# Performance work log

Measured on AMD Instinct MI355X. Metric: run time of the kernel, lower is better.

## Reference

```python
import jax, jax.numpy as jnp
import numpy as np

DN = ('NDHWC', 'DHWIO', 'NDHWC')
EPS = 1e-5  # torch BatchNorm default

def _conv(x, w, s):
    # Minkowski conv, kernel 3 centered: output coord j gathers input coords s*j + {-1,0,1}
    return jax.lax.conv_general_dilated(x, w, (s, s, s), ((1, 1),) * 3, dimension_numbers=DN)

def _convt(x, w):
    # stride-2 transpose conv, kernel 3 centered: output p gets input c where 2c in {p-1,p,p+1}
    return jax.lax.conv_general_dilated(x, w, (1, 1, 1), ((1, 2),) * 3,
                                        lhs_dilation=(2, 2, 2), dimension_numbers=DN)

def _down(m):
    # stride-2 coordinate map: a coarse voxel is active iff any of its 2x2x2 fine voxels is
    B, G = m.shape[0], m.shape[1]
    return m.reshape(B, G // 2, 2, G // 2, 2, G // 2, 2).any(axis=(2, 4, 6))

def _mbn(h, m, g, b):
    # MinkowskiBatchNorm: BatchNorm1d over the active (sparse) feature rows only
    mf = m[..., None].astype(h.dtype)
    h = h * mf
    cnt = jnp.maximum(jnp.sum(mf), 1.0)
    mean = jnp.sum(h, axis=(0, 1, 2, 3)) / cnt
    var = jnp.sum(((h - mean) * mf) ** 2, axis=(0, 1, 2, 3)) / cnt
    return ((h - mean) * jax.lax.rsqrt(var + EPS) * g + b) * mf


def setup_inputs() -> dict:
    key = jax.random.key(0)
    ks = jax.random.split(key, 8)
    B, G, Cin, Cout = 2, 64, 4, 16
    def w(k, shape, fan):
        return jax.random.normal(k, shape, jnp.float32) * np.float32(1.0 / np.sqrt(fan))
    return {
        'x': jax.random.normal(ks[0], (B, G, G, G, Cin), jnp.float32),
        'mask': jax.random.bernoulli(ks[1], 0.1, (B, G, G, G)),
        'w1': w(ks[2], (3, 3, 3, Cin, 8), 27 * Cin), 'g1': jnp.ones(8), 'b1': jnp.zeros(8),
        'w2': w(ks[3], (3, 3, 3, 8, 16), 27 * 8), 'g2': jnp.ones(16), 'b2': jnp.zeros(16),
        'w3': w(ks[4], (3, 3, 3, 16, 32), 27 * 16), 'g3': jnp.ones(32), 'b3': jnp.zeros(32),
        'w3t': w(ks[5], (3, 3, 3, 32, 16), 27 * 32), 'g3t': jnp.ones(16), 'b3t': jnp.zeros(16),
        'w2t': w(ks[6], (3, 3, 3, 32, 16), 27 * 32), 'g2t': jnp.ones(16), 'b2t': jnp.zeros(16),
        'w1x1': w(ks[7], (24, Cout), 24),
    }


def reference(x, mask, w1, g1, b1, w2, g2, b2, w3, g3, b3,
              w3t, g3t, b3t, w2t, g2t, b2t, w1x1):
    m1 = mask
    m2 = _down(m1)
    m4 = _down(m2)
    mf1 = m1[..., None].astype(x.dtype)

    xs = x * mf1                                      # sparse tensor: zero at inactive coords
    s1 = _mbn(_conv(xs, w1, 1), m1, g1, b1)           # block1, stride 1
    o = jax.nn.relu(s1)
    s2 = _mbn(_conv(o, w2, 2), m2, g2, b2)            # block2, stride 2
    o = jax.nn.relu(s2)
    s4 = _mbn(_conv(o, w3, 2), m4, g3, b3)            # block3, stride 4
    o = jax.nn.relu(s4)

    o = jax.nn.relu(_mbn(_convt(o, w3t), m2, g3t, b3t))   # block3_tr -> stride-2 coords
    o = jnp.concatenate([o, s2], axis=-1)                 # ME.cat(out, out_s2) -> 32 ch
    o = jax.nn.relu(_mbn(_convt(o, w2t), m1, g2t, b2t))   # block2_tr -> stride-1 coords
    o = jnp.concatenate([o, s1], axis=-1)                 # ME.cat(out, out_s1) -> 24 ch
    return jnp.einsum('bdhwc,co->bdhwo', o, w1x1) * mf1   # conv1_tr: 1x1x1 conv
```

## Files before the change

kernel.cpp:

```cpp
#include <hip/hip_runtime.h>

#define NVOX1 524288
#define NVOX2 65536
#define NVOX4 8192

#define ST_SUM1 16
#define ST_SQ1  24
#define ST_SUM2 32
#define ST_SQ2  48
#define ST_SUM3 64
#define ST_SQ3  96
#define ST_SUM3T 128
#define ST_SQ3T  144
#define ST_SUM2T 160
#define ST_SQ2T  176
#define FLAG_OFF 200
#define IC_N1 204
#define IC_N2 205
#define IC_N4 206
#define ST_ZERO 256

#define OFF_M1C 512
#define OFF_M2  (OFF_M1C + NVOX1)
#define OFF_M4  (OFF_M2 + NVOX2)
#define OFF_H1  (OFF_M4 + NVOX4)
#define OFF_S2  (OFF_H1 + NVOX1 * 8)
#define OFF_H3  (OFF_S2 + NVOX2 * 16)
#define OFF_T3  (OFF_H3 + NVOX4 * 32)
#define OFF_L1  (OFF_T3 + NVOX2 * 16)
#define OFF_L2  (OFF_L1 + NVOX1)
#define OFF_L4  (OFF_L2 + NVOX2)
#define OFF_BC1 (OFF_L4 + NVOX4)
#define OFF_BC2 (OFF_BC1 + 2048)
#define OFF_BC4 (OFF_BC2 + 256)

#define EPSBN 1e-5f

template <int C>
__device__ __forceinline__ void wreduce(float& a, float& b) {
#pragma unroll
  for (int off = C; off < 64; off <<= 1) {
    a += __shfl_xor(a, off, 64);
    b += __shfl_xor(b, off, 64);
  }
}

__device__ __forceinline__ int taps1d(int p, int gin, int* c, int* k) {
  if ((p & 1) == 0) { c[0] = p >> 1; k[0] = 1; return 1; }
  int n = 0;
  c[n] = (p - 1) >> 1; k[n] = 0; n++;
  int c2 = (p + 1) >> 1;
  if (c2 < gin) { c[n] = c2; k[n] = 2; n++; }
  return n;
}

__global__ __launch_bounds__(256) void k_detect(const unsigned int* __restrict__ m,
                                                int* __restrict__ flags) {
  int tid = blockIdx.x * 256 + threadIdx.x;
  int hasf = 0, hasb = 0;
  for (int i = tid; i < NVOX1; i += 256 * 256) {
    unsigned int v = m[i];
    if (v == 0x3F800000u) hasf = 1;
    else if (v > 1u) hasb = 1;
  }
  hasf = __syncthreads_or(hasf);
  hasb = __syncthreads_or(hasb);
  if (threadIdx.x == 0) {
    if (hasf) atomicOr(&flags[0], 1);
    if (hasb) atomicOr(&flags[1], 1);
  }
}

__global__ __launch_bounds__(256) void k_canon(const void* __restrict__ mraw,
                                               int* __restrict__ m1c,
                                               const int* __restrict__ flags,
                                               int* __restrict__ blkcnt1) {
  int idx = blockIdx.x * 256 + threadIdx.x;
  int isf = flags[0], isb = flags[1];
  int v;
  if (isf)      v = (((const float*)mraw)[idx] != 0.f);
  else if (isb) v = (((const unsigned char*)mraw)[idx] != 0);
  else          v = (((const int*)mraw)[idx] != 0);
  m1c[idx] = v;
  int c = __syncthreads_count(v);
  if (threadIdx.x == 0) blkcnt1[blockIdx.x] = c;
}

__global__ __launch_bounds__(256) void k_down1(const int* __restrict__ m1,
                                               int* __restrict__ m2,
                                               int* __restrict__ blkcnt2) {
  int idx = blockIdx.x * 256 + threadIdx.x;
  int x = idx & 31, y = (idx >> 5) & 31, z = (idx >> 10) & 31, b = idx >> 15;
  int any = 0;
#pragma unroll
  for (int dz = 0; dz < 2; dz++)
#pragma unroll
    for (int dy = 0; dy < 2; dy++)
#pragma unroll
      for (int dx = 0; dx < 2; dx++)
        any |= m1[((b * 64 + 2 * z + dz) * 64 + 2 * y + dy) * 64 + 2 * x + dx];
  any = any ? 1 : 0;
  m2[idx] = any;
  int c = __syncthreads_count(any);
  if (threadIdx.x == 0) blkcnt2[blockIdx.x] = c;
}

__global__ __launch_bounds__(256) void k_down2(const int* __restrict__ m2,
                                               int* __restrict__ m4,
                                               int* __restrict__ blkcnt4) {
  int idx = blockIdx.x * 256 + threadIdx.x;
  int x = idx & 15, y = (idx >> 4) & 15, z = (idx >> 8) & 15, b = idx >> 12;
  int any = 0;
#pragma unroll
  for (int dz = 0; dz < 2; dz++)
#pragma unroll
    for (int dy = 0; dy < 2; dy++)
#pragma unroll
      for (int dx = 0; dx < 2; dx++)
        any |= m2[((b * 32 + 2 * z + dz) * 32 + 2 * y + dy) * 32 + 2 * x + dx];
  any = any ? 1 : 0;
  m4[idx] = any;
  int c = __syncthreads_count(any);
  if (threadIdx.x == 0) blkcnt4[blockIdx.x] = c;
}

__global__ __launch_bounds__(1024) void k_scan(int* __restrict__ bc1,
                                               int* __restrict__ bc2,
                                               int* __restrict__ bc4,
                                               int* __restrict__ cnts) {
  __shared__ int sA[2048], sB[2048];
  int* a; int n; int outIdx;
  if (blockIdx.x == 0)      { a = bc1; n = 2048; outIdx = IC_N1; }
  else if (blockIdx.x == 1) { a = bc2; n = 256;  outIdx = IC_N2; }
  else                      { a = bc4; n = 32;   outIdx = IC_N4; }
  int t = threadIdx.x;
  int i0 = t, i1 = t + 1024;
  int v0 = (i0 < n) ? a[i0] : 0;
  int v1 = (i1 < n) ? a[i1] : 0;
  sA[i0] = v0; sA[i1] = v1;
  __syncthreads();
  int* src = sA; int* dst = sB;
  for (int st = 1; st < 2048; st <<= 1) {
    int x0 = src[i0]; if (i0 >= st) x0 += src[i0 - st];
    int x1 = src[i1]; if (i1 >= st) x1 += src[i1 - st];
    dst[i0] = x0; dst[i1] = x1;
    __syncthreads();
    int* tmp = src; src = dst; dst = tmp;
  }
  if (i0 < n) a[i0] = src[i0] - v0;
  if (i1 < n) a[i1] = src[i1] - v1;
  if (t == 0) cnts[outIdx] = src[2047];
}

__global__ __launch_bounds__(256) void k_scatter(const int* __restrict__ m1,
                                                 const int* __restrict__ m2,
                                                 const int* __restrict__ m4,
                                                 const int* __restrict__ bc1,
                                                 const int* __restrict__ bc2,
                                                 const int* __restrict__ bc4,
                                                 int* __restrict__ list1,
                                                 int* __restrict__ list2,
                                                 int* __restrict__ list4) {
  __shared__ int s_w[4];
  int bid = blockIdx.x, t = threadIdx.x;
  const int* mask; const int* base; int* list; int lb;
  if (bid < 2048)      { mask = m1; base = bc1; list = list1; lb = bid; }
  else if (bid < 2304) { mask = m2; base = bc2; list = list2; lb = bid - 2048; }
  else                 { mask = m4; base = bc4; list = list4; lb = bid - 2304; }
  int idx = lb * 256 + t;
  int act = mask[idx];
  unsigned long long b = __ballot(act != 0);
  int lane = t & 63, wid = t >> 6;
  if (lane == 0) s_w[wid] = __popcll(b);
  __syncthreads();
  int wbase = 0;
  for (int i = 0; i < wid; i++) wbase += s_w[i];
  if (act) {
    int pre = __popcll(b & ((1ull << lane) - 1ull));
    list[base[lb] + wbase + pre] = idx;
  }
}

__global__ __launch_bounds__(256) void k_conv1(const float* __restrict__ x,
                                               const int* __restrict__ m1,
                                               const int* __restrict__ list1,
                                               const int* __restrict__ cnts,
                                               const float* __restrict__ w,
                                               float* __restrict__ h1,
                                               float* __restrict__ stats) {
  __shared__ float s_w[27 * 36];
  __shared__ float s_sum[8], s_sq[8];
  int t = threadIdx.x;
  { const float4* w4 = (const float4*)w;
    for (int i = t; i < 216; i += 256) {
      int flat = i * 4, tap = flat >> 5, rem = flat & 31;
      *(float4*)(s_w + tap * 36 + rem) = w4[i];
    } }
  if (t < 8) { s_sum[t] = 0.f; s_sq[t] = 0.f; }
  __syncthreads();
  int items = cnts[IC_N1] * 8;
  float sum = 0.f, sq = 0.f;
  for (int i = blockIdx.x * 256 + t; i < items; i += gridDim.x * 256) {
    int li = i >> 3, co = i & 7;
    int v = list1[li];
    int vx = v & 63, vy = (v >> 6) & 63, vz = (v >> 12) & 63, vb = v >> 18;
    float a0 = 0.f, a1 = 0.f;
    for (int kd = 0; kd < 3; kd++) { int d = vz + kd - 1; if ((unsigned)d >= 64u) continue;
      for (int kh = 0; kh < 3; kh++) { int h = vy + kh - 1; if ((unsigned)h >= 64u) continue;
        for (int kw = 0; kw < 3; kw++) { int ww = vx + kw - 1; if ((unsigned)ww >= 64u) continue;
          int ni = ((vb * 64 + d) * 64 + h) * 64 + ww;
          if (!m1[ni]) continue;
          float4 ip = *(const float4*)(x + (size_t)ni * 4);
          const float* wp = s_w + ((kd * 3 + kh) * 3 + kw) * 36 + co;
          a0 = fmaf(ip.x, wp[0], a0);
          a1 = fmaf(ip.y, wp[8], a1);
          a0 = fmaf(ip.z, wp[16], a0);
          a1 = fmaf(ip.w, wp[24], a1);
        } } }
    float acc = a0 + a1;
    h1[(size_t)v * 8 + co] = acc;
    sum += acc; sq += acc * acc;
  }
  wreduce<8>(sum, sq);
  if ((t & 63) < 8) { atomicAdd(&s_sum[t & 7], sum); atomicAdd(&s_sq[t & 7], sq); }
  __syncthreads();
  if (t < 8) {
    if (s_sum[t] != 0.f) atomicAdd(&stats[ST_SUM1 + t], s_sum[t]);
    if (s_sq[t]  != 0.f) atomicAdd(&stats[ST_SQ1 + t], s_sq[t]);
  }
}

__global__ __launch_bounds__(256) void k_conv2(const float* __restrict__ h1,
                                               const int* __restrict__ m1,
                                               const int* __restrict__ list2,
                                               const int* __restrict__ cnts,
                                               const float* __restrict__ w,
                                               const float* __restrict__ g1,
                                               const float* __restrict__ b1,
                                               float* __restrict__ s2,
                                               float* __restrict__ stats) {
  __shared__ float s_w[27 * 132];
  __shared__ float s_sc[8], s_bi[8];
  __shared__ float s_sum[16], s_sq[16];
  int t = threadIdx.x;
  { const float4* w4 = (const float4*)w;
    for (int i = t; i < 864; i += 256) {
      int flat = i * 4, tap = flat >> 7, rem = flat & 127;
      *(float4*)(s_w + tap * 132 + rem) = w4[i];
    } }
  if (t < 8) {
    float cnt = fmaxf((float)cnts[IC_N1], 1.f);
    float mean = stats[ST_SUM1 + t] / cnt;
    float var = fmaxf(stats[ST_SQ1 + t] / cnt - mean * mean, 0.f);
    float sc = g1[t] * rsqrtf(var + EPSBN);
    s_sc[t] = sc; s_bi[t] = b1[t] - mean * sc;
  }
  if (t < 16) { s_sum[t] = 0.f; s_sq[t] = 0.f; }
  __syncthreads();
  int items = cnts[IC_N2] * 16;
  float sum = 0.f, sq = 0.f;
  for (int i = blockIdx.x * 256 + t; i < items; i += gridDim.x * 256) {
    int li = i >> 4, co = i & 15;
    int v = list2[li];
    int vx = v & 31, vy = (v >> 5) & 31, vz = (v >> 10) & 31, vb = v >> 15;
    float a0 = 0.f, a1 = 0.f;
    for (int kd = 0; kd < 3; kd++) { int d = 2 * vz + kd - 1; if ((unsigned)d >= 64u) continue;
      for (int kh = 0; kh < 3; kh++) { int h = 2 * vy + kh - 1; if ((unsigned)h >= 64u) continue;
        for (int kw = 0; kw < 3; kw++) { int ww = 2 * vx + kw - 1; if ((unsigned)ww >= 64u) continue;
          int ni = ((vb * 64 + d) * 64 + h) * 64 + ww;
          if (!m1[ni]) continue;
          float4 i0 = *(const float4*)(h1 + (size_t)ni * 8);
          float4 i1 = *(const float4*)(h1 + (size_t)ni * 8 + 4);
          const float* wp = s_w + ((kd * 3 + kh) * 3 + kw) * 132 + co;
          float vv;
          vv = fmaxf(fmaf(i0.x, s_sc[0], s_bi[0]), 0.f); a0 = fmaf(vv, wp[0 * 16], a0);
          vv = fmaxf(fmaf(i0.y, s_sc[1], s_bi[1]), 0.f); a1 = fmaf(vv, wp[1 * 16], a1);
          vv = fmaxf(fmaf(i0.z, s_sc[2], s_bi[2]), 0.f); a0 = fmaf(vv, wp[2 * 16], a0);
          vv = fmaxf(fmaf(i0.w, s_sc[3], s_bi[3]), 0.f); a1 = fmaf(vv, wp[3 * 16], a1);
          vv = fmaxf(fmaf(i1.x, s_sc[4], s_bi[4]), 0.f); a0 = fmaf(vv, wp[4 * 16], a0);
          vv = fmaxf(fmaf(i1.y, s_sc[5], s_bi[5]), 0.f); a1 = fmaf(vv, wp[5 * 16], a1);
          vv = fmaxf(fmaf(i1.z, s_sc[6], s_bi[6]), 0.f); a0 = fmaf(vv, wp[6 * 16], a0);
          vv = fmaxf(fmaf(i1.w, s_sc[7], s_bi[7]), 0.f); a1 = fmaf(vv, wp[7 * 16], a1);
        } } }
    float acc = a0 + a1;
    s2[(size_t)v * 16 + co] = acc;
    sum += acc; sq += acc * acc;
  }
  wreduce<16>(sum, sq);
  if ((t & 63) < 16) { atomicAdd(&s_sum[t & 15], sum); atomicAdd(&s_sq[t & 15], sq); }
  __syncthreads();
  if (t < 16) {
    if (s_sum[t] != 0.f) atomicAdd(&stats[ST_SUM2 + t], s_sum[t]);
    if (s_sq[t]  != 0.f) atomicAdd(&stats[ST_SQ2 + t], s_sq[t]);
  }
}

__global__ __launch_bounds__(512) void k_conv3(const float* __restrict__ s2raw,
                                               const int* __restrict__ m2,
                                               const int* __restrict__ list4,
                                               const int* __restrict__ cnts,
                                               const float* __restrict__ w,
                                               const float* __restrict__ g2,
                                               const float* __restrict__ b2,
                                               float* __restrict__ h3,
                                               float* __restrict__ stats) {
  __shared__ float s_w[27 * 516];
  __shared__ float s_sc[16], s_bi[16];
  __shared__ float s_sum[32], s_sq[32];
  int t = threadIdx.x;
  { const float4* w4 = (const float4*)w;
    for (int i = t; i < 3456; i += 512) {
      int flat = i * 4, tap = flat >> 9, rem = flat & 511;
      *(float4*)(s_w + tap * 516 + rem) = w4[i];
    } }
  if (t < 16) {
    float cnt = fmaxf((float)cnts[IC_N2], 1.f);
    float mean = stats[ST_SUM2 + t] / cnt;
    float var = fmaxf(stats[ST_SQ2 + t] / cnt - mean * mean, 0.f);
    float sc = g2[t] * rsqrtf(var + EPSBN);
    s_sc[t] = sc; s_bi[t] = b2[t] - mean * sc;
  }
  if (t < 32) { s_sum[t] = 0.f; s_sq[t] = 0.f; }
  __syncthreads();
  int items = cnts[IC_N4] * 32;
  float sum = 0.f, sq = 0.f;
  for (int i = blockIdx.x * 512 + t; i < items; i += gridDim.x * 512) {
    int li = i >> 5, co = i & 31;
    int v = list4[li];
    int vx = v & 15, vy = (v >> 4) & 15, vz = (v >> 8) & 15, vb = v >> 12;
    float ac[4] = {0.f, 0.f, 0.f, 0.f};
    for (int kd = 0; kd < 3; kd++) { int d = 2 * vz + kd - 1; if ((unsigned)d >= 32u) continue;
      for (int kh = 0; kh < 3; kh++) { int h = 2 * vy + kh - 1; if ((unsigned)h >= 32u) continue;
        for (int kw = 0; kw < 3; kw++) { int ww = 2 * vx + kw - 1; if ((unsigned)ww >= 32u) continue;
          int ni = ((vb * 32 + d) * 32 + h) * 32 + ww;
          if (!m2[ni]) continue;
          const float4* ip = (const float4*)(s2raw + (size_t)ni * 16);
          const float* wp = s_w + ((kd * 3 + kh) * 3 + kw) * 516 + co;
#pragma unroll
          for (int cq = 0; cq < 4; cq++) {
            float4 q = ip[cq];
            float vv;
            vv = fmaxf(fmaf(q.x, s_sc[cq * 4 + 0], s_bi[cq * 4 + 0]), 0.f); ac[0] = fmaf(vv, wp[(cq * 4 + 0) * 32], ac[0]);
            vv = fmaxf(fmaf(q.y, s_sc[cq * 4 + 1], s_bi[cq * 4 + 1]), 0.f); ac[1] = fmaf(vv, wp[(cq * 4 + 1) * 32], ac[1]);
            vv = fmaxf(fmaf(q.z, s_sc[cq * 4 + 2], s_bi[cq * 4 + 2]), 0.f); ac[2] = fmaf(vv, wp[(cq * 4 + 2) * 32], ac[2]);
            vv = fmaxf(fmaf(q.w, s_sc[cq * 4 + 3], s_bi[cq * 4 + 3]), 0.f); ac[3] = fmaf(vv, wp[(cq * 4 + 3) * 32], ac[3]);
          }
        } } }
    float acc = (ac[0] + ac[1]) + (ac[2] + ac[3]);
    h3[(size_t)v * 32 + co] = acc;
    sum += acc; sq += acc * acc;
  }
  wreduce<32>(sum, sq);
  if ((t & 63) < 32) { atomicAdd(&s_sum[t & 31], sum); atomicAdd(&s_sq[t & 31], sq); }
  __syncthreads();
  if (t < 32) {
    if (s_sum[t] != 0.f) atomicAdd(&stats[ST_SUM3 + t], s_sum[t]);
    if (s_sq[t]  != 0.f) atomicAdd(&stats[ST_SQ3 + t], s_sq[t]);
  }
}

__global__ __launch_bounds__(512) void k_convt3(const float* __restrict__ h3raw,
                                                const int* __restrict__ m4,
                                                const int* __restrict__ list2,
                                                const int* __restrict__ cnts,
                                                const float* __restrict__ w,
                                                const float* __restrict__ g3,
                                                const float* __restrict__ b3,
                                                float* __restrict__ t3,
                                                float* __restrict__ stats) {
  __shared__ float s_w[27 * 516];
  __shared__ float s_sc[32], s_bi[32];
  __shared__ float s_sum[16], s_sq[16];
  int t = threadIdx.x;
  { const float4* w4 = (const float4*)w;
    for (int i = t; i < 3456; i += 512) {
      int flat = i * 4, tap = flat >> 9, rem = flat & 511;
      *(float4*)(s_w + tap * 516 + rem) = w4[i];
    } }
  if (t < 32) {
    float cnt = fmaxf((float)cnts[IC_N4], 1.f);
    float mean = stats[ST_SUM3 + t] / cnt;
    float var = fmaxf(stats[ST_SQ3 + t] / cnt - mean * mean, 0.f);
    float sc = g3[t] * rsqrtf(var + EPSBN);
    s_sc[t] = sc; s_bi[t] = b3[t] - mean * sc;
  }
  if (t < 16) { s_sum[t] = 0.f; s_sq[t] = 0.f; }
  __syncthreads();
  int items = cnts[IC_N2] * 16;
  float sum = 0.f, sq = 0.f;
  for (int i = blockIdx.x * 512 + t; i < items; i += gridDim.x * 512) {
    int li = i >> 4, co = i & 15;
    int v = list2[li];
    int px = v & 31, py = (v >> 5) & 31, pz = (v >> 10) & 31, vb = v >> 15;
    int cz[2], kz[2], cy[2], ky[2], cx[2], kx[2];
    int nz = taps1d(pz, 16, cz, kz);
    int ny = taps1d(py, 16, cy, ky);
    int nx = taps1d(px, 16, cx, kx);
    float ac[4] = {0.f, 0.f, 0.f, 0.f};
    for (int iz = 0; iz < nz; iz++)
      for (int iy = 0; iy < ny; iy++)
        for (int ix = 0; ix < nx; ix++) {
          int ni = ((vb * 16 + cz[iz]) * 16 + cy[iy]) * 16 + cx[ix];
          if (!m4[ni]) continue;
          const float4* ip = (const float4*)(h3raw + (size_t)ni * 32);
          const float* wp = s_w + ((kz[iz] * 3 + ky[iy]) * 3 + kx[ix]) * 516 + co;
#pragma unroll
          for (int cq = 0; cq < 8; cq++) {
            float4 q = ip[cq];
            float vv;
            vv = fmaxf(fmaf(q.x, s_sc[cq * 4 + 0], s_bi[cq * 4 + 0]), 0.f); ac[0] = fmaf(vv, wp[(cq * 4 + 0) * 16], ac[0]);
            vv = fmaxf(fmaf(q.y, s_sc[cq * 4 + 1], s_bi[cq * 4 + 1]), 0.f); ac[1] = fmaf(vv, wp[(cq * 4 + 1) * 16], ac[1]);
            vv = fmaxf(fmaf(q.z, s_sc[cq * 4 + 2], s_bi[cq * 4 + 2]), 0.f); ac[2] = fmaf(vv, wp[(cq * 4 + 2) * 16], ac[2]);
            vv = fmaxf(fmaf(q.w, s_sc[cq * 4 + 3], s_bi[cq * 4 + 3]), 0.f); ac[3] = fmaf(vv, wp[(cq * 4 + 3) * 16], ac[3]);
          }
        }
    float acc = (ac[0] + ac[1]) + (ac[2] + ac[3]);
    t3[(size_t)v * 16 + co] = acc;
    sum += acc; sq += acc * acc;
  }
  wreduce<16>(sum, sq);
  if ((t & 63) < 16) { atomicAdd(&s_sum[t & 15], sum); atomicAdd(&s_sq[t & 15], sq); }
  __syncthreads();
  if (t < 16) {
    if (s_sum[t] != 0.f) atomicAdd(&stats[ST_SUM3T + t], s_sum[t]);
    if (s_sq[t]  != 0.f) atomicAdd(&stats[ST_SQ3T + t], s_sq[t]);
  }
}

__global__ __launch_bounds__(512) void k_convt2(const float* __restrict__ t3raw,
                                                const float* __restrict__ s2raw,
                                                const int* __restrict__ m2,
                                                const int* __restrict__ list1,
                                                const int* __restrict__ cnts,
                                                const float* __restrict__ w,
                                                const float* __restrict__ g3t,
                                                const float* __restrict__ b3t,
                                                const float* __restrict__ g2,
                                                const float* __restrict__ b2,
                                                float* __restrict__ outraw,
                                                float* __restrict__ stats) {
  __shared__ float s_w[27 * 516];
  __shared__ float s_sct[16], s_bit[16], s_sc2[16], s_bi2[16];
  __shared__ float s_sum[16], s_sq[16];
  int t = threadIdx.x;
  { const float4* w4 = (const float4*)w;
    for (int i = t; i < 3456; i += 512) {
      int flat = i * 4, tap = flat >> 9, rem = flat & 511;
      *(float4*)(s_w + tap * 516 + rem) = w4[i];
    } }
  if (t < 16) {
    float cnt = fmaxf((float)cnts[IC_N2], 1.f);
    float mean = stats[ST_SUM3T + t] / cnt;
    float var = fmaxf(stats[ST_SQ3T + t] / cnt - mean * mean, 0.f);
    float sc = g3t[t] * rsqrtf(var + EPSBN);
    s_sct[t] = sc; s_bit[t] = b3t[t] - mean * sc;
    float mean2 = stats[ST_SUM2 + t] / cnt;
    float var2 = fmaxf(stats[ST_SQ2 + t] / cnt - mean2 * mean2, 0.f);
    float sc2 = g2[t] * rsqrtf(var2 + EPSBN);
    s_sc2[t] = sc2; s_bi2[t] = b2[t] - mean2 * sc2;
    s_sum[t] = 0.f; s_sq[t] = 0.f;
  }
  __syncthreads();
  int items = cnts[IC_N1] * 16;
  float sum = 0.f, sq = 0.f;
  for (int i = blockIdx.x * 512 + t; i < items; i += gridDim.x * 512) {
    int li = i >> 4, co = i & 15;
    int v = list1[li];
    int px = v & 63, py = (v >> 6) & 63, pz = (v >> 12) & 63, vb = v >> 18;
    int cz[2], kz[2], cy[2], ky[2], cx[2], kx[2];
    int nz = taps1d(pz, 32, cz, kz);
    int ny = taps1d(py, 32, cy, ky);
    int nx = taps1d(px, 32, cx, kx);
    float ac[4] = {0.f, 0.f, 0.f, 0.f};
    for (int iz = 0; iz < nz; iz++)
      for (int iy = 0; iy < ny; iy++)
        for (int ix = 0; ix < nx; ix++) {
          int ni = ((vb * 32 + cz[iz]) * 32 + cy[iy]) * 32 + cx[ix];
          if (!m2[ni]) continue;
          const float4* tp = (const float4*)(t3raw + (size_t)ni * 16);
          const float4* sp = (const float4*)(s2raw + (size_t)ni * 16);
          const float* wp = s_w + ((kz[iz] * 3 + ky[iy]) * 3 + kx[ix]) * 516 + co;
#pragma unroll
          for (int cq = 0; cq < 4; cq++) {
            float4 q = tp[cq];
            float vv;
            vv = fmaxf(fmaf(q.x, s_sct[cq * 4 + 0], s_bit[cq * 4 + 0]), 0.f); ac[0] = fmaf(vv, wp[(cq * 4 + 0) * 16], ac[0]);
            vv = fmaxf(fmaf(q.y, s_sct[cq * 4 + 1], s_bit[cq * 4 + 1]), 0.f); ac[1] = fmaf(vv, wp[(cq * 4 + 1) * 16], ac[1]);
            vv = fmaxf(fmaf(q.z, s_sct[cq * 4 + 2], s_bit[cq * 4 + 2]), 0.f); ac[2] = fmaf(vv, wp[(cq * 4 + 2) * 16], ac[2]);
            vv = fmaxf(fmaf(q.w, s_sct[cq * 4 + 3], s_bit[cq * 4 + 3]), 0.f); ac[3] = fmaf(vv, wp[(cq * 4 + 3) * 16], ac[3]);
          }
#pragma unroll
          for (int cq = 0; cq < 4; cq++) {
            float4 q = sp[cq];
            float vv;
            vv = fmaf(q.x, s_sc2[cq * 4 + 0], s_bi2[cq * 4 + 0]); ac[0] = fmaf(vv, wp[(16 + cq * 4 + 0) * 16], ac[0]);
            vv = fmaf(q.y, s_sc2[cq * 4 + 1], s_bi2[cq * 4 + 1]); ac[1] = fmaf(vv, wp[(16 + cq * 4 + 1) * 16], ac[1]);
            vv = fmaf(q.z, s_sc2[cq * 4 + 2], s_bi2[cq * 4 + 2]); ac[2] = fmaf(vv, wp[(16 + cq * 4 + 2) * 16], ac[2]);
            vv = fmaf(q.w, s_sc2[cq * 4 + 3], s_bi2[cq * 4 + 3]); ac[3] = fmaf(vv, wp[(16 + cq * 4 + 3) * 16], ac[3]);
          }
        }
    float acc = (ac[0] + ac[1]) + (ac[2] + ac[3]);
    outraw[(size_t)v * 16 + co] = acc;
    sum += acc; sq += acc * acc;
  }
  wreduce<16>(sum, sq);
  if ((t & 63) < 16) { atomicAdd(&s_sum[t & 15], sum); atomicAdd(&s_sq[t & 15], sq); }
  __syncthreads();
  if (t < 16) {
    if (s_sum[t] != 0.f) atomicAdd(&stats[ST_SUM2T + t], s_sum[t]);
    if (s_sq[t]  != 0.f) atomicAdd(&stats[ST_SQ2T + t], s_sq[t]);
  }
}

__global__ __launch_bounds__(256) void k_final(float* __restrict__ out,
                                               const float* __restrict__ h1raw,
                                               const int* __restrict__ list1,
                                               const int* __restrict__ cnts,
                                               const float* __restrict__ g2t,
                                               const float* __restrict__ b2t,
                                               const float* __restrict__ g1,
                                               const float* __restrict__ b1,
                                               const float* __restrict__ w1x1,
                                               const float* __restrict__ stats) {
  __shared__ float s_sc[16], s_bi[16], s_sc1[8], s_bi1[8], s_w[384];
  int t = threadIdx.x;
  for (int i = t; i < 384; i += 256) s_w[i] = w1x1[i];
  if (t < 16) {
    float cnt = fmaxf((float)cnts[IC_N1], 1.f);
    float mean = stats[ST_SUM2T + t] / cnt;
    float var = fmaxf(stats[ST_SQ2T + t] / cnt - mean * mean, 0.f);
    float sc = g2t[t] * rsqrtf(var + EPSBN);
    s_sc[t] = sc; s_bi[t] = b2t[t] - mean * sc;
  }
  if (t < 8) {
    float cnt = fmaxf((float)cnts[IC_N1], 1.f);
    float mean = stats[ST_SUM1 + t] / cnt;
    float var = fmaxf(stats[ST_SQ1 + t] / cnt - mean * mean, 0.f);
    float sc = g1[t] * rsqrtf(var + EPSBN);
    s_sc1[t] = sc; s_bi1[t] = b1[t] - mean * sc;
  }
  __syncthreads();
  int n = cnts[IC_N1];
  for (int i = blockIdx.x * 256 + t; i < n; i += gridDim.x * 256) {
    int v = list1[i];
    float* op = out + (size_t)v * 16;
    float t2[16];
    {
      const float4* op4 = (const float4*)op;
#pragma unroll
      for (int cq = 0; cq < 4; cq++) {
        float4 q = op4[cq];
        t2[cq * 4 + 0] = fmaxf(fmaf(q.x, s_sc[cq * 4 + 0], s_bi[cq * 4 + 0]), 0.f);
        t2[cq * 4 + 1] = fmaxf(fmaf(q.y, s_sc[cq * 4 + 1], s_bi[cq * 4 + 1]), 0.f);
        t2[cq * 4 + 2] = fmaxf(fmaf(q.z, s_sc[cq * 4 + 2], s_bi[cq * 4 + 2]), 0.f);
        t2[cq * 4 + 3] = fmaxf(fmaf(q.w, s_sc[cq * 4 + 3], s_bi[cq * 4 + 3]), 0.f);
      }
    }
    float s1v[8];
    {
      const float4* sp4 = (const float4*)(h1raw + (size_t)v * 8);
#pragma unroll
      for (int cq = 0; cq < 2; cq++) {
        float4 q = sp4[cq];
        s1v[cq * 4 + 0] = fmaf(q.x, s_sc1[cq * 4 + 0], s_bi1[cq * 4 + 0]);
        s1v[cq * 4 + 1] = fmaf(q.y, s_sc1[cq * 4 + 1], s_bi1[cq * 4 + 1]);
        s1v[cq * 4 + 2] = fmaf(q.z, s_sc1[cq * 4 + 2], s_bi1[cq * 4 + 2]);
        s1v[cq * 4 + 3] = fmaf(q.w, s_sc1[cq * 4 + 3], s_bi1[cq * 4 + 3]);
      }
    }
    float o[16];
#pragma unroll
    for (int oc = 0; oc < 16; oc++) o[oc] = 0.f;
#pragma unroll
    for (int c = 0; c < 16; c++) {
      float vv = t2[c];
#pragma unroll
      for (int oc = 0; oc < 16; oc++) o[oc] = fmaf(vv, s_w[c * 16 + oc], o[oc]);
    }
#pragma unroll
    for (int c = 0; c < 8; c++) {
      float vv = s1v[c];
#pragma unroll
      for (int oc = 0; oc < 16; oc++) o[oc] = fmaf(vv, s_w[(16 + c) * 16 + oc], o[oc]);
    }
    float4* op4 = (float4*)op;
#pragma unroll
    for (int cq = 0; cq < 4; cq++) {
      float4 q = {o[cq * 4 + 0], o[cq * 4 + 1], o[cq * 4 + 2], o[cq * 4 + 3]};
      op4[cq] = q;
    }
  }
}

extern "C" void kernel_launch(void* const* d_in, const int* in_sizes, int n_in,
                              void* d_out, int out_size, void* d_ws, size_t ws_size,
                              hipStream_t stream) {
  const float* x    = (const float*)d_in[0];
  const void*  mraw = d_in[1];
  const float* w1   = (const float*)d_in[2];
  const float* g1   = (const float*)d_in[3];
  const float* b1   = (const float*)d_in[4];
  const float* w2   = (const float*)d_in[5];
  const float* g2   = (const float*)d_in[6];
  const float* b2   = (const float*)d_in[7];
  const float* w3   = (const float*)d_in[8];
  const float* g3   = (const float*)d_in[9];
  const float* b3   = (const float*)d_in[10];
  const float* w3t  = (const float*)d_in[11];
  const float* g3t  = (const float*)d_in[12];
  const float* b3t  = (const float*)d_in[13];
  const float* w2t  = (const float*)d_in[14];
  const float* g2t  = (const float*)d_in[15];
  const float* b2t  = (const float*)d_in[16];
  const float* w1x1 = (const float*)d_in[17];

  float* ws = (float*)d_ws;
  float* stats = ws;
  int* cnts = (int*)ws;
  int* flags = (int*)(ws + FLAG_OFF);
  int* m1c = (int*)(ws + OFF_M1C);
  int* m2  = (int*)(ws + OFF_M2);
  int* m4  = (int*)(ws + OFF_M4);
  float* h1 = ws + OFF_H1;
  float* s2 = ws + OFF_S2;
  float* h3 = ws + OFF_H3;
  float* t3 = ws + OFF_T3;
  int* list1 = (int*)(ws + OFF_L1);
  int* list2 = (int*)(ws + OFF_L2);
  int* list4 = (int*)(ws + OFF_L4);
  int* bc1 = (int*)(ws + OFF_BC1);
  int* bc2 = (int*)(ws + OFF_BC2);
  int* bc4 = (int*)(ws + OFF_BC4);
  float* out = (float*)d_out;

  hipMemsetAsync(ws, 0, ST_ZERO * sizeof(float), stream);
  hipMemsetAsync(d_out, 0, (size_t)out_size * sizeof(float), stream);
  k_detect<<<256, 256, 0, stream>>>((const unsigned int*)mraw, flags);
  k_canon<<<NVOX1 / 256, 256, 0, stream>>>(mraw, m1c, flags, bc1);
  k_down1<<<NVOX2 / 256, 256, 0, stream>>>(m1c, m2, bc2);
  k_down2<<<NVOX4 / 256, 256, 0, stream>>>(m2, m4, bc4);
  k_scan<<<3, 1024, 0, stream>>>(bc1, bc2, bc4, cnts);
  k_scatter<<<2048 + 256 + 32, 256, 0, stream>>>(m1c, m2, m4, bc1, bc2, bc4, list1, list2, list4);
  k_conv1<<<1024, 256, 0, stream>>>(x, m1c, list1, cnts, w1, h1, stats);
  k_conv2<<<1024, 256, 0, stream>>>(h1, m1c, list2, cnts, w2, g1, b1, s2, stats);
  k_conv3<<<512, 512, 0, stream>>>(s2, m2, list4, cnts, w3, g2, b2, h3, stats);
  k_convt3<<<512, 512, 0, stream>>>(h3, m4, list2, cnts, w3t, g3, b3, t3, stats);
  k_convt2<<<512, 512, 0, stream>>>(t3, s2, m2, list1, cnts, w2t, g3t, b3t, g2, b2, out, stats);
  k_final<<<256, 256, 0, stream>>>(out, h1, list1, cnts, g2t, b2t, g1, b1, w1x1, stats);
}
```

Baseline: 238.7 us.

## Make sparse conv gathers branchless with mask multiplies and fully unrolled taps

Replaces the data-dependent `continue` on inactive or out-of-range neighbours in all five conv kernels with fully unrolled tap loops. Each tap now always loads its neighbour (clamped index) and scales the partial sum by a 0/1 mask factor. The transpose convs use fixed two-tap lists per axis with zero weights for missing taps. The goal is to remove wavefront divergence and let the compiler batch independent loads. The cost is that every tap now loads memory and does the arithmetic even when about 90% of neighbours are inactive. The shared-memory weight padding (stride 36/132/516) is also removed in favour of a plain contiguous copy, which may reintroduce LDS bank conflicts.

```diff
diff --git a/kernel.cpp b/kernel.cpp
--- a/kernel.cpp
+++ b/kernel.cpp
@@ -45,13 +45,11 @@
   }
 }
 
-__device__ __forceinline__ int taps1d(int p, int gin, int* c, int* k) {
-  if ((p & 1) == 0) { c[0] = p >> 1; k[0] = 1; return 1; }
-  int n = 0;
-  c[n] = (p - 1) >> 1; k[n] = 0; n++;
-  int c2 = (p + 1) >> 1;
-  if (c2 < gin) { c[n] = c2; k[n] = 2; n++; }
-  return n;
+__device__ __forceinline__ void ttaps(int p, int gin, int* c, int* k, float* f) {
+  c[0] = p >> 1; k[0] = (p & 1) ? 0 : 1; f[0] = 1.f;
+  int cb = (p + 1) >> 1;
+  int ok = (p & 1) && (cb < gin);
+  c[1] = ok ? cb : 0; k[1] = 2; f[1] = ok ? 1.f : 0.f;
 }
 
 __global__ __launch_bounds__(256) void k_detect(const unsigned int* __restrict__ m,
@@ -188,14 +186,11 @@
                                                const float* __restrict__ w,
                                                float* __restrict__ h1,
                                                float* __restrict__ stats) {
-  __shared__ float s_w[27 * 36];
+  __shared__ float s_w[27 * 32];
   __shared__ float s_sum[8], s_sq[8];
   int t = threadIdx.x;
-  { const float4* w4 = (const float4*)w;
-    for (int i = t; i < 216; i += 256) {
-      int flat = i * 4, tap = flat >> 5, rem = flat & 31;
-      *(float4*)(s_w + tap * 36 + rem) = w4[i];
-    } }
+  { const float4* w4 = (const float4*)w; float4* sw4 = (float4*)s_w;
+    for (int i = t; i < 216; i += 256) sw4[i] = w4[i]; }
   if (t < 8) { s_sum[t] = 0.f; s_sq[t] = 0.f; }
   __syncthreads();
   int items = cnts[IC_N1] * 8;
@@ -205,17 +200,24 @@
     int v = list1[li];
     int vx = v & 63, vy = (v >> 6) & 63, vz = (v >> 12) & 63, vb = v >> 18;
     float a0 = 0.f, a1 = 0.f;
-    for (int kd = 0; kd < 3; kd++) { int d = vz + kd - 1; if ((unsigned)d >= 64u) continue;
-      for (int kh = 0; kh < 3; kh++) { int h = vy + kh - 1; if ((unsigned)h >= 64u) continue;
-        for (int kw = 0; kw < 3; kw++) { int ww = vx + kw - 1; if ((unsigned)ww >= 64u) continue;
-          int ni = ((vb * 64 + d) * 64 + h) * 64 + ww;
-          if (!m1[ni]) continue;
+#pragma unroll
+    for (int kd = 0; kd < 3; kd++) {
+      int d = vz + kd - 1; int okd = ((unsigned)d < 64u); int dc = okd ? d : 0;
+#pragma unroll
+      for (int kh = 0; kh < 3; kh++) {
+        int h = vy + kh - 1; int okh = ((unsigned)h < 64u); int hc = okh ? h : 0;
+#pragma unroll
+        for (int kw = 0; kw < 3; kw++) {
+          int ww = vx + kw - 1; int okw = ((unsigned)ww < 64u); int wc = okw ? ww : 0;
+          int ni = ((vb * 64 + dc) * 64 + hc) * 64 + wc;
+          float mf = (float)((okd & okh & okw) * m1[ni]);
           float4 ip = *(const float4*)(x + (size_t)ni * 4);
-          const float* wp = s_w + ((kd * 3 + kh) * 3 + kw) * 36 + co;
-          a0 = fmaf(ip.x, wp[0], a0);
-          a1 = fmaf(ip.y, wp[8], a1);
-          a0 = fmaf(ip.z, wp[16], a0);
-          a1 = fmaf(ip.w, wp[24], a1);
+          const float* wp = s_w + ((kd * 3 + kh) * 3 + kw) * 32 + co;
+          float tac = ip.x * wp[0];
+          tac = fmaf(ip.y, wp[8], tac);
+          tac = fmaf(ip.z, wp[16], tac);
+          tac = fmaf(ip.w, wp[24], tac);
+          a0 = fmaf(mf, tac, a0);
         } } }
     float acc = a0 + a1;
     h1[(size_t)v * 8 + co] = acc;
@@ -239,15 +241,12 @@
                                                const float* __restrict__ b1,
                                                float* __restrict__ s2,
                                                float* __restrict__ stats) {
-  __shared__ float s_w[27 * 132];
+  __shared__ float s_w[27 * 128];
   __shared__ float s_sc[8], s_bi[8];
   __shared__ float s_sum[16], s_sq[16];
   int t = threadIdx.x;
-  { const float4* w4 = (const float4*)w;
-    for (int i = t; i < 864; i += 256) {
-      int flat = i * 4, tap = flat >> 7, rem = flat & 127;
-      *(float4*)(s_w + tap * 132 + rem) = w4[i];
-    } }
+  { const float4* w4 = (const float4*)w; float4* sw4 = (float4*)s_w;
+    for (int i = t; i < 864; i += 256) sw4[i] = w4[i]; }
   if (t < 8) {
     float cnt = fmaxf((float)cnts[IC_N1], 1.f);
     float mean = stats[ST_SUM1 + t] / cnt;
@@ -264,23 +263,31 @@
     int v = list2[li];
     int vx = v & 31, vy = (v >> 5) & 31, vz = (v >> 10) & 31, vb = v >> 15;
     float a0 = 0.f, a1 = 0.f;
-    for (int kd = 0; kd < 3; kd++) { int d = 2 * vz + kd - 1; if ((unsigned)d >= 64u) continue;
-      for (int kh = 0; kh < 3; kh++) { int h = 2 * vy + kh - 1; if ((unsigned)h >= 64u) continue;
-        for (int kw = 0; kw < 3; kw++) { int ww = 2 * vx + kw - 1; if ((unsigned)ww >= 64u) continue;
-          int ni = ((vb * 64 + d) * 64 + h) * 64 + ww;
-          if (!m1[ni]) continue;
+#pragma unroll
+    for (int kd = 0; kd < 3; kd++) {
+      int d = 2 * vz + kd - 1; int okd = (d >= 0); int dc = okd ? d : 0;
+#pragma unroll
+      for (int kh = 0; kh < 3; kh++) {
+        int h = 2 * vy + kh - 1; int okh = (h >= 0); int hc = okh ? h : 0;
+#pragma unroll
+        for (int kw = 0; kw < 3; kw++) {
+          int ww = 2 * vx + kw - 1; int okw = (ww >= 0); int wc = okw ? ww : 0;
+          int ni = ((vb * 64 + dc) * 64 + hc) * 64 + wc;
+          float mf = (float)((okd & okh & okw) * m1[ni]);
           float4 i0 = *(const float4*)(h1 + (size_t)ni * 8);
           float4 i1 = *(const float4*)(h1 + (size_t)ni * 8 + 4);
-          const float* wp = s_w + ((kd * 3 + kh) * 3 + kw) * 132 + co;
-          float vv;
-          vv = fmaxf(fmaf(i0.x, s_sc[0], s_bi[0]), 0.f); a0 = fmaf(vv, wp[0 * 16], a0);
-          vv = fmaxf(fmaf(i0.y, s_sc[1], s_bi[1]), 0.f); a1 = fmaf(vv, wp[1 * 16], a1);
-          vv = fmaxf(fmaf(i0.z, s_sc[2], s_bi[2]), 0.f); a0 = fmaf(vv, wp[2 * 16], a0);
-          vv = fmaxf(fmaf(i0.w, s_sc[3], s_bi[3]), 0.f); a1 = fmaf(vv, wp[3 * 16], a1);
-          vv = fmaxf(fmaf(i1.x, s_sc[4], s_bi[4]), 0.f); a0 = fmaf(vv, wp[4 * 16], a0);
-          vv = fmaxf(fmaf(i1.y, s_sc[5], s_bi[5]), 0.f); a1 = fmaf(vv, wp[5 * 16], a1);
-          vv = fmaxf(fmaf(i1.z, s_sc[6], s_bi[6]), 0.f); a0 = fmaf(vv, wp[6 * 16], a0);
-          vv = fmaxf(fmaf(i1.w, s_sc[7], s_bi[7]), 0.f); a1 = fmaf(vv, wp[7 * 16], a1);
+          const float* wp = s_w + ((kd * 3 + kh) * 3 + kw) * 128 + co;
+          float t0 = 0.f, t1 = 0.f, vv;
+          vv = fmaxf(fmaf(i0.x, s_sc[0], s_bi[0]), 0.f); t0 = fmaf(vv, wp[0 * 16], t0);
+          vv = fmaxf(fmaf(i0.y, s_sc[1], s_bi[1]), 0.f); t1 = fmaf(vv, wp[1 * 16], t1);
+          vv = fmaxf(fmaf(i0.z, s_sc[2], s_bi[2]), 0.f); t0 = fmaf(vv, wp[2 * 16], t0);
+          vv = fmaxf(fmaf(i0.w, s_sc[3], s_bi[3]), 0.f); t1 = fmaf(vv, wp[3 * 16], t1);
+          vv = fmaxf(fmaf(i1.x, s_sc[4], s_bi[4]), 0.f); t0 = fmaf(vv, wp[4 * 16], t0);
+          vv = fmaxf(fmaf(i1.y, s_sc[5], s_bi[5]), 0.f); t1 = fmaf(vv, wp[5 * 16], t1);
+          vv = fmaxf(fmaf(i1.z, s_sc[6], s_bi[6]), 0.f); t0 = fmaf(vv, wp[6 * 16], t0);
+          vv = fmaxf(fmaf(i1.w, s_sc[7], s_bi[7]), 0.f); t1 = fmaf(vv, wp[7 * 16], t1);
+          a0 = fmaf(mf, t0, a0);
+          a1 = fmaf(mf, t1, a1);
         } } }
     float acc = a0 + a1;
     s2[(size_t)v * 16 + co] = acc;
@@ -304,15 +311,12 @@
                                                const float* __restrict__ b2,
                                                float* __restrict__ h3,
                                                float* __restrict__ stats) {
-  __shared__ float s_w[27 * 516];
+  __shared__ float s_w[27 * 512];
   __shared__ float s_sc[16], s_bi[16];
   __shared__ float s_sum[32], s_sq[32];
   int t = threadIdx.x;
-  { const float4* w4 = (const float4*)w;
-    for (int i = t; i < 3456; i += 512) {
-      int flat = i * 4, tap = flat >> 9, rem = flat & 511;
-      *(float4*)(s_w + tap * 516 + rem) = w4[i];
-    } }
+  { const float4* w4 = (const float4*)w; float4* sw4 = (float4*)s_w;
+    for (int i = t; i < 3456; i += 512) sw4[i] = w4[i]; }
   if (t < 16) {
     float cnt = fmaxf((float)cnts[IC_N2], 1.f);
     float mean = stats[ST_SUM2 + t] / cnt;
@@ -328,25 +332,34 @@
     int li = i >> 5, co = i & 31;
     int v = list4[li];
     int vx = v & 15, vy = (v >> 4) & 15, vz = (v >> 8) & 15, vb = v >> 12;
-    float ac[4] = {0.f, 0.f, 0.f, 0.f};
-    for (int kd = 0; kd < 3; kd++) { int d = 2 * vz + kd - 1; if ((unsigned)d >= 32u) continue;
-      for (int kh = 0; kh < 3; kh++) { int h = 2 * vy + kh - 1; if ((unsigned)h >= 32u) continue;
-        for (int kw = 0; kw < 3; kw++) { int ww = 2 * vx + kw - 1; if ((unsigned)ww >= 32u) continue;
-          int ni = ((vb * 32 + d) * 32 + h) * 32 + ww;
-          if (!m2[ni]) continue;
+    float a0 = 0.f, a1 = 0.f;
+#pragma unroll
+    for (int kd = 0; kd < 3; kd++) {
+      int d = 2 * vz + kd - 1; int okd = (d >= 0); int dc = okd ? d : 0;
+#pragma unroll
+      for (int kh = 0; kh < 3; kh++) {
+        int h = 2 * vy + kh - 1; int okh = (h >= 0); int hc = okh ? h : 0;
+#pragma unroll
+        for (int kw = 0; kw < 3; kw++) {
+          int ww = 2 * vx + kw - 1; int okw = (ww >= 0); int wc = okw ? ww : 0;
+          int ni = ((vb * 32 + dc) * 32 + hc) * 32 + wc;
+          float mf = (float)((okd & okh & okw) * m2[ni]);
           const float4* ip = (const float4*)(s2raw + (size_t)ni * 16);
-          const float* wp = s_w + ((kd * 3 + kh) * 3 + kw) * 516 + co;
+          const float* wp = s_w + ((kd * 3 + kh) * 3 + kw) * 512 + co;
+          float t0 = 0.f, t1 = 0.f;
 #pragma unroll
           for (int cq = 0; cq < 4; cq++) {
             float4 q = ip[cq];
             float vv;
-            vv = fmaxf(fmaf(q.x, s_sc[cq * 4 + 0], s_bi[cq * 4 + 0]), 0.f); ac[0] = fmaf(vv, wp[(cq * 4 + 0) * 32], ac[0]);
-            vv = fmaxf(fmaf(q.y, s_sc[cq * 4 + 1], s_bi[cq * 4 + 1]), 0.f); ac[1] = fmaf(vv, wp[(cq * 4 + 1) * 32], ac[1]);
-            vv = fmaxf(fmaf(q.z, s_sc[cq * 4 + 2], s_bi[cq * 4 + 2]), 0.f); ac[2] = fmaf(vv, wp[(cq * 4 + 2) * 32], ac[2]);
-            vv = fmaxf(fmaf(q.w, s_sc[cq * 4 + 3], s_bi[cq * 4 + 3]), 0.f); ac[3] = fmaf(vv, wp[(cq * 4 + 3) * 32], ac[3]);
+            vv = fmaxf(fmaf(q.x, s_sc[cq * 4 + 0], s_bi[cq * 4 + 0]), 0.f); t0 = fmaf(vv, wp[(cq * 4 + 0) * 32], t0);
+            vv = fmaxf(fmaf(q.y, s_sc[cq * 4 + 1], s_bi[cq * 4 + 1]), 0.f); t1 = fmaf(vv, wp[(cq * 4 + 1) * 32], t1);
+            vv = fmaxf(fmaf(q.z, s_sc[cq * 4 + 2], s_bi[cq * 4 + 2]), 0.f); t0 = fmaf(vv, wp[(cq * 4 + 2) * 32], t0);
+            vv = fmaxf(fmaf(q.w, s_sc[cq * 4 + 3], s_bi[cq * 4 + 3]), 0.f); t1 = fmaf(vv, wp[(cq * 4 + 3) * 32], t1);
           }
+          a0 = fmaf(mf, t0, a0);
+          a1 = fmaf(mf, t1, a1);
         } } }
-    float acc = (ac[0] + ac[1]) + (ac[2] + ac[3]);
+    float acc = a0 + a1;
     h3[(size_t)v * 32 + co] = acc;
     sum += acc; sq += acc * acc;
   }
@@ -368,15 +381,12 @@
                                                 const float* __restrict__ b3,
                                                 float* __restrict__ t3,
                                                 float* __restrict__ stats) {
-  __shared__ float s_w[27 * 516];
+  __shared__ float s_w[27 * 512];
   __shared__ float s_sc[32], s_bi[32];
   __shared__ float s_sum[16], s_sq[16];
   int t = threadIdx.x;
-  { const float4* w4 = (const float4*)w;
-    for (int i = t; i < 3456; i += 512) {
-      int flat = i * 4, tap = flat >> 9, rem = flat & 511;
-      *(float4*)(s_w + tap * 516 + rem) = w4[i];
-    } }
+  { const float4* w4 = (const float4*)w; float4* sw4 = (float4*)s_w;
+    for (int i = t; i < 3456; i += 512) sw4[i] = w4[i]; }
   if (t < 32) {
     float cnt = fmaxf((float)cnts[IC_N4], 1.f);
     float mean = stats[ST_SUM3 + t] / cnt;
@@ -392,29 +402,37 @@
     int li = i >> 4, co = i & 15;
     int v = list2[li];
     int px = v & 31, py = (v >> 5) & 31, pz = (v >> 10) & 31, vb = v >> 15;
-    int cz[2], kz[2], cy[2], ky[2], cx[2], kx[2];
-    int nz = taps1d(pz, 16, cz, kz);
-    int ny = taps1d(py, 16, cy, ky);
-    int nx = taps1d(px, 16, cx, kx);
-    float ac[4] = {0.f, 0.f, 0.f, 0.f};
-    for (int iz = 0; iz < nz; iz++)
-      for (int iy = 0; iy < ny; iy++)
-        for (int ix = 0; ix < nx; ix++) {
-          int ni = ((vb * 16 + cz[iz]) * 16 + cy[iy]) * 16 + cx[ix];
-          if (!m4[ni]) continue;
+    int czv[2], kzv[2], cyv[2], kyv[2], cxv[2], kxv[2];
+    float fzv[2], fyv[2], fxv[2];
+    ttaps(pz, 16, czv, kzv, fzv);
+    ttaps(py, 16, cyv, kyv, fyv);
+    ttaps(px, 16, cxv, kxv, fxv);
+    float a0 = 0.f, a1 = 0.f, a2 = 0.f, a3 = 0.f;
+#pragma unroll
+    for (int dz = 0; dz < 2; dz++)
+#pragma unroll
+      for (int dy = 0; dy < 2; dy++)
+#pragma unroll
+        for (int dx = 0; dx < 2; dx++) {
+          float f = fzv[dz] * fyv[dy] * fxv[dx];
+          int ni = ((vb * 16 + czv[dz]) * 16 + cyv[dy]) * 16 + cxv[dx];
+          float mf = f * (float)m4[ni];
           const float4* ip = (const float4*)(h3raw + (size_t)ni * 32);
-          const float* wp = s_w + ((kz[iz] * 3 + ky[iy]) * 3 + kx[ix]) * 516 + co;
+          const float* wp = s_w + ((kzv[dz] * 3 + kyv[dy]) * 3 + kxv[dx]) * 512 + co;
+          float t0 = 0.f, t1 = 0.f, t2 = 0.f, t3a = 0.f;
 #pragma unroll
           for (int cq = 0; cq < 8; cq++) {
             float4 q = ip[cq];
             float vv;
-            vv = fmaxf(fmaf(q.x, s_sc[cq * 4 + 0], s_bi[cq * 4 + 0]), 0.f); ac[0] = fmaf(vv, wp[(cq * 4 + 0) * 16], ac[0]);
-            vv = fmaxf(fmaf(q.y, s_sc[cq * 4 + 1], s_bi[cq * 4 + 1]), 0.f); ac[1] = fmaf(vv, wp[(cq * 4 + 1) * 16], ac[1]);
-            vv = fmaxf(fmaf(q.z, s_sc[cq * 4 + 2], s_bi[cq * 4 + 2]), 0.f); ac[2] = fmaf(vv, wp[(cq * 4 + 2) * 16], ac[2]);
-            vv = fmaxf(fmaf(q.w, s_sc[cq * 4 + 3], s_bi[cq * 4 + 3]), 0.f); ac[3] = fmaf(vv, wp[(cq * 4 + 3) * 16], ac[3]);
+            vv = fmaxf(fmaf(q.x, s_sc[cq * 4 + 0], s_bi[cq * 4 + 0]), 0.f); t0 = fmaf(vv, wp[(cq * 4 + 0) * 16], t0);
+            vv = fmaxf(fmaf(q.y, s_sc[cq * 4 + 1], s_bi[cq * 4 + 1]), 0.f); t1 = fmaf(vv, wp[(cq * 4 + 1) * 16], t1);
+            vv = fmaxf(fmaf(q.z, s_sc[cq * 4 + 2], s_bi[cq * 4 + 2]), 0.f); t2 = fmaf(vv, wp[(cq * 4 + 2) * 16], t2);
+            vv = fmaxf(fmaf(q.w, s_sc[cq * 4 + 3], s_bi[cq * 4 + 3]), 0.f); t3a = fmaf(vv, wp[(cq * 4 + 3) * 16], t3a);
           }
+          a0 = fmaf(mf, t0, a0); a1 = fmaf(mf, t1, a1);
+          a2 = fmaf(mf, t2, a2); a3 = fmaf(mf, t3a, a3);
         }
-    float acc = (ac[0] + ac[1]) + (ac[2] + ac[3]);
+    float acc = (a0 + a1) + (a2 + a3);
     t3[(size_t)v * 16 + co] = acc;
     sum += acc; sq += acc * acc;
   }
@@ -439,15 +457,12 @@
                                                 const float* __restrict__ b2,
                                                 float* __restrict__ outraw,
                                                 float* __restrict__ stats) {
-  __shared__ float s_w[27 * 516];
+  __shared__ float s_w[27 * 512];
   __shared__ float s_sct[16], s_bit[16], s_sc2[16], s_bi2[16];
   __shared__ float s_sum[16], s_sq[16];
   int t = threadIdx.x;
-  { const float4* w4 = (const float4*)w;
-    for (int i = t; i < 3456; i += 512) {
-      int flat = i * 4, tap = flat >> 9, rem = flat & 511;
-      *(float4*)(s_w + tap * 516 + rem) = w4[i];
-    } }
+  { const float4* w4 = (const float4*)w; float4* sw4 = (float4*)s_w;
+    for (int i = t; i < 3456; i += 512) sw4[i] = w4[i]; }
   if (t < 16) {
     float cnt = fmaxf((float)cnts[IC_N2], 1.f);
     float mean = stats[ST_SUM3T + t] / cnt;
@@ -467,39 +482,47 @@
     int li = i >> 4, co = i & 15;
     int v = list1[li];
     int px = v & 63, py = (v >> 6) & 63, pz = (v >> 12) & 63, vb = v >> 18;
-    int cz[2], kz[2], cy[2], ky[2], cx[2], kx[2];
-    int nz = taps1d(pz, 32, cz, kz);
-    int ny = taps1d(py, 32, cy, ky);
-    int nx = taps1d(px, 32, cx, kx);
-    float ac[4] = {0.f, 0.f, 0.f, 0.f};
-    for (int iz = 0; iz < nz; iz++)
-      for (int iy = 0; iy < ny; iy++)
-        for (int ix = 0; ix < nx; ix++) {
-          int ni = ((vb * 32 + cz[iz]) * 32 + cy[iy]) * 32 + cx[ix];
-          if (!m2[ni]) continue;
+    int czv[2], kzv[2], cyv[2], kyv[2], cxv[2], kxv[2];
+    float fzv[2], fyv[2], fxv[2];
+    ttaps(pz, 32, czv, kzv, fzv);
+    ttaps(py, 32, cyv, kyv, fyv);
+    ttaps(px, 32, cxv, kxv, fxv);
+    float a0 = 0.f, a1 = 0.f, a2 = 0.f, a3 = 0.f;
+#pragma unroll
+    for (int dz = 0; dz < 2; dz++)
+#pragma unroll
+      for (int dy = 0; dy < 2; dy++)
+#pragma unroll
+        for (int dx = 0; dx < 2; dx++) {
+          float f = fzv[dz] * fyv[dy] * fxv[dx];
+          int ni = ((vb * 32 + czv[dz]) * 32 + cyv[dy]) * 32 + cxv[dx];
+          float mf = f * (float)m2[ni];
           const float4* tp = (const float4*)(t3raw + (size_t)ni * 16);
           const float4* sp = (const float4*)(s2raw + (size_t)ni * 16);
-          const float* wp = s_w + ((kz[iz] * 3 + ky[iy]) * 3 + kx[ix]) * 516 + co;
+          const float* wp = s_w + ((kzv[dz] * 3 + kyv[dy]) * 3 + kxv[dx]) * 512 + co;
+          float t0 = 0.f, t1 = 0.f, t2 = 0.f, t3a = 0.f;
 #pragma unroll
           for (int cq = 0; cq < 4; cq++) {
             float4 q = tp[cq];
             float vv;
-            vv = fmaxf(fmaf(q.x, s_sct[cq * 4 + 0], s_bit[cq * 4 + 0]), 0.f); ac[0] = fmaf(vv, wp[(cq * 4 + 0) * 16], ac[0]);
-            vv = fmaxf(fmaf(q.y, s_sct[cq * 4 + 1], s_bit[cq * 4 + 1]), 0.f); ac[1] = fmaf(vv, wp[(cq * 4 + 1) * 16], ac[1]);
-            vv = fmaxf(fmaf(q.z, s_sct[cq * 4 + 2], s_bit[cq * 4 + 2]), 0.f); ac[2] = fmaf(vv, wp[(cq * 4 + 2) * 16], ac[2]);
-            vv = fmaxf(fmaf(q.w, s_sct[cq * 4 + 3], s_bit[cq * 4 + 3]), 0.f); ac[3] = fmaf(vv, wp[(cq * 4 + 3) * 16], ac[3]);
+            vv = fmaxf(fmaf(q.x, s_sct[cq * 4 + 0], s_bit[cq * 4 + 0]), 0.f); t0 = fmaf(vv, wp[(cq * 4 + 0) * 16], t0);
+            vv = fmaxf(fmaf(q.y, s_sct[cq * 4 + 1], s_bit[cq * 4 + 1]), 0.f); t1 = fmaf(vv, wp[(cq * 4 + 1) * 16], t1);
+            vv = fmaxf(fmaf(q.z, s_sct[cq * 4 + 2], s_bit[cq * 4 + 2]), 0.f); t0 = fmaf(vv, wp[(cq * 4 + 2) * 16], t0);
+            vv = fmaxf(fmaf(q.w, s_sct[cq * 4 + 3], s_bit[cq * 4 + 3]), 0.f); t1 = fmaf(vv, wp[(cq * 4 + 3) * 16], t1);
           }
 #pragma unroll
           for (int cq = 0; cq < 4; cq++) {
             float4 q = sp[cq];
             float vv;
-            vv = fmaf(q.x, s_sc2[cq * 4 + 0], s_bi2[cq * 4 + 0]); ac[0] = fmaf(vv, wp[(16 + cq * 4 + 0) * 16], ac[0]);
-            vv = fmaf(q.y, s_sc2[cq * 4 + 1], s_bi2[cq * 4 + 1]); ac[1] = fmaf(vv, wp[(16 + cq * 4 + 1) * 16], ac[1]);
-            vv = fmaf(q.z, s_sc2[cq * 4 + 2], s_bi2[cq * 4 + 2]); ac[2] = fmaf(vv, wp[(16 + cq * 4 + 2) * 16], ac[2]);
-            vv = fmaf(q.w, s_sc2[cq * 4 + 3], s_bi2[cq * 4 + 3]); ac[3] = fmaf(vv, wp[(16 + cq * 4 + 3) * 16], ac[3]);
+            vv = fmaf(q.x, s_sc2[cq * 4 + 0], s_bi2[cq * 4 + 0]); t2 = fmaf(vv, wp[(16 + cq * 4 + 0) * 16], t2);
+            vv = fmaf(q.y, s_sc2[cq * 4 + 1], s_bi2[cq * 4 + 1]); t3a = fmaf(vv, wp[(16 + cq * 4 + 1) * 16], t3a);
+            vv = fmaf(q.z, s_sc2[cq * 4 + 2], s_bi2[cq * 4 + 2]); t2 = fmaf(vv, wp[(16 + cq * 4 + 2) * 16], t2);
+            vv = fmaf(q.w, s_sc2[cq * 4 + 3], s_bi2[cq * 4 + 3]); t3a = fmaf(vv, wp[(16 + cq * 4 + 3) * 16], t3a);
           }
+          a0 = fmaf(mf, t0, a0); a1 = fmaf(mf, t1, a1);
+          a2 = fmaf(mf, t2, a2); a3 = fmaf(mf, t3a, a3);
         }
-    float acc = (ac[0] + ac[1]) + (ac[2] + ac[3]);
+    float acc = (a0 + a1) + (a2 + a3);
     outraw[(size_t)v * 16 + co] = acc;
     sum += acc; sq += acc * acc;
   }
```

Result: slower. 510.5 us (+113.9%).
